# Kernel optimization log

Measured on AMD Instinct MI355X. Metric: run time of the kernel, lower is better.

## Reference

```python
import jax, jax.numpy as jnp
import numpy as np

T, B, D = 2048, 1, 1024
N_HEAD, D_HEAD, D_FF = 16, 64, 4096
LN_EPS = 1e-5


def layer_norm(x, g, b):
    m = jnp.mean(x, axis=-1, keepdims=True)
    v = jnp.mean(jnp.square(x - m), axis=-1, keepdims=True)
    return (x - m) * jax.lax.rsqrt(v + LN_EPS) * g + b


def rel_shift(x):
    # x: (qlen, klen, bsz, n_head) -> Transformer-XL relative shift
    q, k, b, h = x.shape
    zp = jnp.zeros((q, 1, b, h), dtype=x.dtype)
    x = jnp.concatenate([zp, x], axis=1)            # (q, k+1, b, h)
    x = x.reshape(k + 1, q, b, h)[1:].reshape(q, k, b, h)
    return x


def setup_inputs() -> dict:
    key = jax.random.key(0)
    ks = jax.random.split(key, 12)
    s = lambda fan: 1.0 / np.sqrt(fan)
    inp = {
        "input": jax.random.normal(ks[0], (T, B, D), jnp.float32),
        "pos": jax.random.normal(ks[1], (T, 1, D), jnp.float32),
        "r_w_bias": jax.random.normal(ks[2], (N_HEAD, D_HEAD), jnp.float32) * 0.02,
        "r_r_bias": jax.random.normal(ks[3], (N_HEAD, D_HEAD), jnp.float32) * 0.02,
        # causal mask: True = masked (future positions)
        "mask": jnp.triu(jnp.ones((T, T), dtype=bool), k=1),
        "ln1_g": jnp.ones((D,), jnp.float32),
        "ln1_b": jnp.zeros((D,), jnp.float32),
        "qkv_w": jax.random.normal(ks[4], (D, 3 * D), jnp.float32) * s(D),
        "r_w": jax.random.normal(ks[5], (D, D), jnp.float32) * s(D),
        "o_w": jax.random.normal(ks[6], (D, D), jnp.float32) * s(D),
        "ln2_g": jnp.ones((D,), jnp.float32),
        "ln2_b": jnp.zeros((D,), jnp.float32),
        "ff_w1": jax.random.normal(ks[7], (D, D_FF), jnp.float32) * s(D),
        "ff_b1": jnp.zeros((D_FF,), jnp.float32),
        "ff_w2": jax.random.normal(ks[8], (D_FF, D), jnp.float32) * s(D_FF),
        "ff_b2": jnp.zeros((D,), jnp.float32),
    }
    return inp


def reference(input, pos, r_w_bias, r_r_bias, mask, ln1_g, ln1_b, qkv_w, r_w,
              o_w, ln2_g, ln2_b, ff_w1, ff_b1, ff_w2, ff_b2):
    scale = 1.0 / np.sqrt(D_HEAD)
    # preprocess_attn: layernorm
    q_in = layer_norm(input, ln1_g, ln1_b)                      # (T,B,D)
    w_heads = jnp.einsum('tbd,de->tbe', q_in, qkv_w)            # (T,B,3D)
    w_q, w_k, w_v = jnp.split(w_heads, 3, axis=-1)
    w_q = w_q.reshape(T, B, N_HEAD, D_HEAD)
    w_k = w_k.reshape(T, B, N_HEAD, D_HEAD)
    w_v = w_v.reshape(T, B, N_HEAD, D_HEAD)
    r_k = (pos[:, 0] @ r_w).reshape(T, N_HEAD, D_HEAD)          # (T,h,dh)

    AC = jnp.einsum('ibnd,jbnd->ijbn', w_q + r_w_bias, w_k)     # (T,T,B,h)
    BD = rel_shift(jnp.einsum('ibnd,jnd->ijbn', w_q + r_r_bias, r_k))
    score = (AC + BD) * scale
    score = jnp.where(mask[:, :, None, None], jnp.finfo(score.dtype).min, score)
    probs = jax.nn.softmax(score, axis=1)                       # coverage
    attn_vec = jnp.einsum('ijbn,jbnd->ibnd', probs, w_v).reshape(T, B, D)
    attn_out = jnp.einsum('tbd,de->tbe', attn_vec, o_w)
    # postprocess_attn: (dropout=identity) + residual
    x = input + attn_out
    # FFN block: layernorm > linear-relu-linear > residual
    y = layer_norm(x, ln2_g, ln2_b)
    y = jax.nn.relu(jnp.einsum('tbd,df->tbf', y, ff_w1) + ff_b1)
    y = jnp.einsum('tbf,fd->tbd', y, ff_w2) + ff_b2
    x = x + y
    return x, probs
```

## Files before the change

kernel.cpp:

```cpp
#include <hip/hip_runtime.h>
#include <hip/hip_bf16.h>
#include <stdint.h>

using bf16 = __hip_bfloat16;
using short8 = __attribute__((ext_vector_type(8))) short;
using f32x4 = __attribute__((ext_vector_type(4))) float;

#define T_SEQ 2048
#define DMODEL 1024
#define NHEAD 16
#define DHEAD 64
#define DFF 4096

struct __align__(8) bf16x4 { bf16 x, y, z, w; };

__device__ __forceinline__ void async_cp16(const bf16* g, bf16* l) {
  __builtin_amdgcn_global_load_lds(
      (const __attribute__((address_space(1))) uint32_t*)g,
      (__attribute__((address_space(3))) uint32_t*)l, 16, 0, 0);
}

__global__ __launch_bounds__(256) void transpose_cvt(const float* __restrict__ src,
                                                     bf16* __restrict__ dst,
                                                     int R, int C) {
  __shared__ float tile[32][33];
  int bx = blockIdx.x * 32;
  int by = blockIdx.y * 32;
  int tx = threadIdx.x, ty = threadIdx.y;
#pragma unroll
  for (int r = 0; r < 32; r += 8)
    tile[ty + r][tx] = src[(long)(by + ty + r) * C + bx + tx];
  __syncthreads();
#pragma unroll
  for (int r = 0; r < 32; r += 8)
    dst[(long)(bx + ty + r) * R + by + tx] = __float2bfloat16(tile[tx][ty + r]);
}

__global__ __launch_bounds__(256) void cvt_bf16(const float* __restrict__ src,
                                                bf16* __restrict__ dst, int n4) {
  int idx = blockIdx.x * 256 + threadIdx.x;
  if (idx < n4) {
    float4 v = ((const float4*)src)[idx];
    bf16x4 o{__float2bfloat16(v.x), __float2bfloat16(v.y),
             __float2bfloat16(v.z), __float2bfloat16(v.w)};
    ((bf16x4*)dst)[idx] = o;
  }
}

__global__ __launch_bounds__(256) void ln_cvt(const float* __restrict__ x,
                                              const float* __restrict__ g,
                                              const float* __restrict__ b,
                                              bf16* __restrict__ out) {
  int row = blockIdx.x;
  int tid = threadIdx.x;
  float4 v = ((const float4*)(x + (long)row * DMODEL))[tid];
  float s = v.x + v.y + v.z + v.w;
  float s2 = v.x * v.x + v.y * v.y + v.z * v.z + v.w * v.w;
#pragma unroll
  for (int off = 32; off > 0; off >>= 1) {
    s += __shfl_down(s, off);
    s2 += __shfl_down(s2, off);
  }
  __shared__ float ss[4], ss2[4];
  int wave = tid >> 6, lane = tid & 63;
  if (lane == 0) { ss[wave] = s; ss2[wave] = s2; }
  __syncthreads();
  s = ss[0] + ss[1] + ss[2] + ss[3];
  s2 = ss2[0] + ss2[1] + ss2[2] + ss2[3];
  float mean = s * (1.0f / DMODEL);
  float var = s2 * (1.0f / DMODEL) - mean * mean;
  float rstd = rsqrtf(var + 1e-5f);
  float4 gg = ((const float4*)g)[tid];
  float4 bb = ((const float4*)b)[tid];
  bf16x4 o{__float2bfloat16((v.x - mean) * rstd * gg.x + bb.x),
           __float2bfloat16((v.y - mean) * rstd * gg.y + bb.y),
           __float2bfloat16((v.z - mean) * rstd * gg.z + bb.z),
           __float2bfloat16((v.w - mean) * rstd * gg.w + bb.w)};
  ((bf16x4*)(out + (long)row * DMODEL))[tid] = o;
}

template <int BN, class Epi>
__global__ __launch_bounds__(256) void gemm_bt(const bf16* __restrict__ A,
                                               const bf16* __restrict__ Bt,
                                               int M, int N, int K,
                                               long aZstride, long bZstride, Epi epi) {
  constexpr int BM = 128;
  constexpr int BK = 32;
  constexpr int NT = BN / 32;
  __shared__ bf16 As[BM * BK];
  __shared__ bf16 Bs[BN * BK];

  const int bm = blockIdx.y, bn = blockIdx.x, z = blockIdx.z;
  const bf16* Ab = A + (long)z * aZstride;
  const bf16* Bb = Bt + (long)z * bZstride;

  const int tid = threadIdx.x;
  const int lane = tid & 63;
  const int wave = tid >> 6;
  const int wr = wave >> 1;
  const int wc = wave & 1;
  const int kEnd = epi.kmax(bm, bn, K);

  const f32x4 zero4 = {0.f, 0.f, 0.f, 0.f};
  f32x4 acc[4][NT];
#pragma unroll
  for (int mt = 0; mt < 4; ++mt)
#pragma unroll
    for (int nt = 0; nt < NT; ++nt) acc[mt][nt] = zero4;

  const int sr = tid >> 2;
  const int sc = (tid & 3) * 8;
  const bf16* aG0 = Ab + (long)(bm * BM + sr) * K + sc;
  const bf16* aG1 = Ab + (long)(bm * BM + 64 + sr) * K + sc;
  bf16* aL0 = As + tid * 8;
  bf16* aL1 = As + 2048 + tid * 8;
  const bf16* bG0 = Bb + (long)(bn * BN + sr) * K + sc;
  bf16* bL0 = Bs + tid * 8;
  const bf16* bG1 = Bb + (long)(bn * BN + 64 + sr) * K + sc;
  bf16* bL1 = Bs + 2048 + tid * 8;

  const int aRow = wr * 64 + (lane & 15);
  const int bRow = wc * (BN / 2) + (lane & 15);
  const int kq = (lane >> 4) * 8;

  for (int k0 = 0; k0 < kEnd; k0 += BK) {
    __syncthreads();
    async_cp16(aG0, aL0);
    async_cp16(aG1, aL1);
    async_cp16(bG0, bL0);
    if constexpr (BN == 128) async_cp16(bG1, bL1);
    aG0 += BK; aG1 += BK; bG0 += BK;
    if constexpr (BN == 128) bG1 += BK;
    __syncthreads();
    short8 af[4], bfr[NT];
#pragma unroll
    for (int mt = 0; mt < 4; ++mt)
      af[mt] = *(const short8*)(As + (aRow + mt * 16) * BK + kq);
#pragma unroll
    for (int nt = 0; nt < NT; ++nt)
      bfr[nt] = *(const short8*)(Bs + (bRow + nt * 16) * BK + kq);
#pragma unroll
    for (int mt = 0; mt < 4; ++mt)
#pragma unroll
      for (int nt = 0; nt < NT; ++nt)
        acc[mt][nt] = __builtin_amdgcn_mfma_f32_16x16x32_bf16(af[mt], bfr[nt],
                                                              acc[mt][nt], 0, 0, 0);
  }

  const int rBase = (lane >> 4) * 4;
  const int cOff = lane & 15;
#pragma unroll
  for (int mt = 0; mt < 4; ++mt) {
#pragma unroll
    for (int nt = 0; nt < NT; ++nt) {
      int row = bm * BM + wr * 64 + mt * 16 + rBase;
      int col = bn * BN + wc * (BN / 2) + nt * 16 + cOff;
      f32x4 v = acc[mt][nt];
#pragma unroll
      for (int r = 0; r < 4; ++r) epi.store(z, row + r, col, v[r]);
    }
  }
}

struct EpiQKV {
  bf16 *Qh, *Kb, *Vt;
  __device__ int kmax(int, int, int K) const { return K; }
  __device__ void store(int, int row, int col, float v) const {
    int n = (col >> 6) & 15, d = col & 63;
    long hoff = ((long)n * T_SEQ + row) * DHEAD + d;
    if (col < DMODEL) {
      Qh[hoff] = __float2bfloat16(v);
    } else if (col < 2 * DMODEL) {
      Kb[hoff] = __float2bfloat16(v);
    } else {
      Vt[((long)n * DHEAD + d) * T_SEQ + row] = __float2bfloat16(v);
    }
  }
};

struct EpiRk {
  bf16* Rk;
  __device__ int kmax(int, int, int K) const { return K; }
  __device__ void store(int, int row, int col, float v) const {
    int n = col >> 6, d = col & 63;
    Rk[((long)n * T_SEQ + row) * DHEAD + d] = __float2bfloat16(v);
  }
};

struct EpiPV {
  bf16* av;
  __device__ int kmax(int bm, int, int K) const {
    int kl = (bm + 1) * 128;
    return kl < K ? kl : K;
  }
  __device__ void store(int z, int row, int col, float v) const {
    av[(long)row * DMODEL + z * DHEAD + col] = __float2bfloat16(v);
  }
};

struct EpiO {
  float* xws;
  const float* inp;
  __device__ int kmax(int, int, int K) const { return K; }
  __device__ void store(int, int row, int col, float v) const {
    long idx = (long)row * DMODEL + col;
    xws[idx] = v + inp[idx];
  }
};

struct EpiFF1 {
  bf16* h;
  const float* b1;
  __device__ int kmax(int, int, int K) const { return K; }
  __device__ void store(int, int row, int col, float v) const {
    h[(long)row * DFF + col] = __float2bfloat16(fmaxf(v + b1[col], 0.f));
  }
};

struct EpiFF2 {
  float* out;
  const float* b2;
  const float* xws;
  __device__ int kmax(int, int, int K) const { return K; }
  __device__ void store(int, int row, int col, float v) const {
    long idx = (long)row * DMODEL + col;
    out[idx] = v + b2[col] + xws[idx];
  }
};

__global__ __launch_bounds__(256) void bias_k(const bf16* __restrict__ Kb,
                                              const bf16* __restrict__ Rk,
                                              const float* __restrict__ rwb,
                                              const float* __restrict__ rrb,
                                              float* __restrict__ acB,
                                              float* __restrict__ rrbR) {
  int idx = blockIdx.x * 256 + threadIdx.x;
  int n = idx >> 11;
  const short8* kp = (const short8*)(Kb + (long)idx * DHEAD);
  const short8* rp = (const short8*)(Rk + (long)idx * DHEAD);
  float s1 = 0.f, s2 = 0.f;
#pragma unroll
  for (int q8 = 0; q8 < 8; ++q8) {
    short8 kv = kp[q8], rv = rp[q8];
#pragma unroll
    for (int e = 0; e < 8; ++e) {
      float w1 = rwb[n * DHEAD + q8 * 8 + e];
      float w2 = rrb[n * DHEAD + q8 * 8 + e];
      s1 += w1 * __bfloat162float(((const bf16*)&kv)[e]);
      s2 += w2 * __bfloat162float(((const bf16*)&rv)[e]);
    }
  }
  acB[idx] = s1;
  rrbR[idx] = s2;
}

__global__ __launch_bounds__(256) void score_k(const bf16* __restrict__ Qh,
                                               const bf16* __restrict__ Kb,
                                               const bf16* __restrict__ Rk,
                                               const float* __restrict__ acB,
                                               const float* __restrict__ rrbR,
                                               bf16* __restrict__ score) {
  const int bn = blockIdx.x, bm = blockIdx.y, z = blockIdx.z;
  if (bn > bm) return;
  __shared__ char smem[65536];
  bf16* Qs  = (bf16*)smem;
  bf16* Ks  = (bf16*)(smem + 16384);
  bf16* Bnd = (bf16*)(smem + 32768);

  const int tid = threadIdx.x;
  const int lane = tid & 63, wave = tid >> 6;
  const int wr = wave >> 1, wc = wave & 1;
  const int kq = (lane >> 4) * 8;
  const int l15 = lane & 15;
  const int base = 128 * (bn - bm) + T_SEQ - 1 - 128;

  const bf16* Qg = Qh + ((long)z * T_SEQ + bm * 128) * DHEAD;
  const bf16* Kg = Kb + ((long)z * T_SEQ + bn * 128) * DHEAD;
  const bf16* Rg = Rk + (long)z * T_SEQ * DHEAD;

#pragma unroll
  for (int it = 0; it < 4; ++it) {
    int s = it * 256 + tid;
    int kh = s >> 9, r = (s >> 2) & 127, c = (s & 3) * 8;
    async_cp16(Qg + (long)r * DHEAD + kh * 32 + c, Qs + s * 8);
    async_cp16(Kg + (long)r * DHEAD + kh * 32 + c, Ks + s * 8);
  }
#pragma unroll
  for (int it = 0; it < 8; ++it) {
    int s = it * 256 + tid;
    int kh = s >> 10, u = (s >> 2) & 255, c = (s & 3) * 8;
    int g = base + u;
    g = g < 0 ? 0 : (g > T_SEQ - 1 ? T_SEQ - 1 : g);
    async_cp16(Rg + (long)g * DHEAD + kh * 32 + c, Bnd + s * 8);
  }

  const f32x4 zero4 = {0.f, 0.f, 0.f, 0.f};
  f32x4 accA[4][4], accW[4][8];
#pragma unroll
  for (int mt = 0; mt < 4; ++mt) {
#pragma unroll
    for (int nt = 0; nt < 4; ++nt) accA[mt][nt] = zero4;
#pragma unroll
    for (int ut = 0; ut < 8; ++ut) accW[mt][ut] = zero4;
  }

  __syncthreads();
#pragma unroll
  for (int kh = 0; kh < 2; ++kh) {
    short8 qa[4], kf[4], wf[8];
#pragma unroll
    for (int mt = 0; mt < 4; ++mt)
      qa[mt] = *(const short8*)(Qs + kh * 4096 + (wr * 64 + mt * 16 + l15) * 32 + kq);
#pragma unroll
    for (int nt = 0; nt < 4; ++nt)
      kf[nt] = *(const short8*)(Ks + kh * 4096 + (wc * 64 + nt * 16 + l15) * 32 + kq);
#pragma unroll
    for (int ut = 0; ut < 8; ++ut)
      wf[ut] = *(const short8*)(Bnd + kh * 8192 + (wc * 128 + ut * 16 + l15) * 32 + kq);
#pragma unroll
    for (int mt = 0; mt < 4; ++mt) {
#pragma unroll
      for (int nt = 0; nt < 4; ++nt)
        accA[mt][nt] = __builtin_amdgcn_mfma_f32_16x16x32_bf16(qa[mt], kf[nt], accA[mt][nt], 0, 0, 0);
#pragma unroll
      for (int ut = 0; ut < 8; ++ut)
        accW[mt][ut] = __builtin_amdgcn_mfma_f32_16x16x32_bf16(qa[mt], wf[ut], accW[mt][ut], 0, 0, 0);
    }
  }
  __syncthreads();

  float wbias[8];
#pragma unroll
  for (int ut = 0; ut < 8; ++ut) {
    int u = wc * 128 + ut * 16 + l15;
    int g = base + u;
    g = g < 0 ? 0 : (g > T_SEQ - 1 ? T_SEQ - 1 : g);
    wbias[ut] = rrbR[(long)z * T_SEQ + g];
  }
  float abias[4];
#pragma unroll
  for (int nt = 0; nt < 4; ++nt)
    abias[nt] = acB[(long)z * T_SEQ + bn * 128 + wc * 64 + nt * 16 + l15];

  bf16* WlH = (bf16*)smem;
  const int quad4 = (lane >> 4) * 4;
  bf16* srow = score + (long)z * T_SEQ * T_SEQ;

  for (int half = 0; half < 2; ++half) {
    if (wr == half) {
#pragma unroll
      for (int mt = 0; mt < 4; ++mt)
#pragma unroll
        for (int ut = 0; ut < 8; ++ut) {
          int lr = mt * 16 + quad4;
          int u = wc * 128 + ut * 16 + l15;
#pragma unroll
          for (int reg = 0; reg < 4; ++reg)
            WlH[(lr + reg) * 272 + u] = __float2bfloat16(accW[mt][ut][reg] + wbias[ut]);
        }
    }
    __syncthreads();
    if (wr == half) {
#pragma unroll
      for (int mt = 0; mt < 4; ++mt)
#pragma unroll
        for (int nt = 0; nt < 4; ++nt) {
          int lr = mt * 16 + quad4;
          int c = wc * 64 + nt * 16 + l15;
#pragma unroll
          for (int reg = 0; reg < 4; ++reg) {
            int r = half * 64 + lr + reg;
            int u = c - r + 128;
            float v = accA[mt][nt][reg] + abias[nt] +
                      __bfloat162float(WlH[(lr + reg) * 272 + u]);
            srow[(long)(bm * 128 + r) * T_SEQ + bn * 128 + c] = __float2bfloat16(v);
          }
        }
    }
    __syncthreads();
  }
}

__global__ __launch_bounds__(256) void softmax_k(const bf16* __restrict__ S,
                                                 float* __restrict__ probs,
                                                 bf16* __restrict__ pb) {
  constexpr int HS = T_SEQ + 8;
  __shared__ bf16 pl[NHEAD * HS];
  __shared__ float rinv_s[NHEAD];
  const int i = blockIdx.x;
  const int tid = threadIdx.x;
  const int wave = tid >> 6, lane = tid & 63;
  const float scale = 0.125f;
  const int nch = ((i + 1) + 511) >> 9;

  for (int q = 0; q < 4; ++q) {
    const int h = wave * 4 + q;
    const bf16* row = S + (long)h * T_SEQ * T_SEQ + (long)i * T_SEQ;
    float m = -1e30f;
    for (int c = 0; c < nch; ++c) {
      int j0 = c * 512 + lane * 8;
      short8 v = *(const short8*)(row + j0);
#pragma unroll
      for (int e = 0; e < 8; ++e) {
        float s = (j0 + e <= i) ? __bfloat162float(((const bf16*)&v)[e]) * scale : -1e30f;
        m = fmaxf(m, s);
      }
    }
#pragma unroll
    for (int off = 1; off < 64; off <<= 1) m = fmaxf(m, __shfl_xor(m, off));
    float l = 0.f;
    for (int c = 0; c < nch; ++c) {
      int j0 = c * 512 + lane * 8;
      short8 v = *(const short8*)(row + j0);
      short8 o;
#pragma unroll
      for (int e = 0; e < 8; ++e) {
        float p = 0.f;
        if (j0 + e <= i) {
          p = __expf(__bfloat162float(((const bf16*)&v)[e]) * scale - m);
          l += p;
        }
        ((bf16*)&o)[e] = __float2bfloat16(p);
      }
      *(short8*)(pl + h * HS + j0) = o;
    }
#pragma unroll
    for (int off = 1; off < 64; off <<= 1) l += __shfl_xor(l, off);
    if (lane == 0) rinv_s[h] = 1.f / l;
  }
  __syncthreads();

  float* prow = probs + (long)i * T_SEQ * NHEAD;
  const int n0 = (tid & 3) * 4;
  float rv0 = rinv_s[n0 + 0], rv1 = rinv_s[n0 + 1];
  float rv2 = rinv_s[n0 + 2], rv3 = rinv_s[n0 + 3];
  for (int it = 0; it < 32; ++it) {
    int o = tid * 4 + it * 1024;
    int j = o >> 4;
    float4 f = {0.f, 0.f, 0.f, 0.f};
    if (j <= i) {
      f.x = __bfloat162float(pl[(n0 + 0) * HS + j]) * rv0;
      f.y = __bfloat162float(pl[(n0 + 1) * HS + j]) * rv1;
      f.z = __bfloat162float(pl[(n0 + 2) * HS + j]) * rv2;
      f.w = __bfloat162float(pl[(n0 + 3) * HS + j]) * rv3;
    }
    ((float4*)prow)[tid + it * 256] = f;
  }

  const int kround = ((i >> 7) + 1) << 7;
  for (int q = 0; q < 4; ++q) {
    const int h = wave * 4 + q;
    bf16* prow_b = pb + (long)h * T_SEQ * T_SEQ + (long)i * T_SEQ;
    float rinv = rinv_s[h];
    for (int j0 = lane * 8; j0 < kround; j0 += 512) {
      short8 v = *(const short8*)(pl + h * HS + j0);
      short8 o;
#pragma unroll
      for (int e = 0; e < 8; ++e)
        ((bf16*)&o)[e] = __float2bfloat16(__bfloat162float(((const bf16*)&v)[e]) * rinv);
      *(short8*)(prow_b + j0) = o;
    }
  }
}

extern "C" void kernel_launch(void* const* d_in, const int* in_sizes, int n_in,
                              void* d_out, int out_size, void* d_ws, size_t ws_size,
                              hipStream_t stream) {
  const float* input = (const float*)d_in[0];
  const float* pos   = (const float*)d_in[1];
  const float* rwb   = (const float*)d_in[2];
  const float* rrb   = (const float*)d_in[3];
  const float* ln1g  = (const float*)d_in[5];
  const float* ln1b  = (const float*)d_in[6];
  const float* qkvw  = (const float*)d_in[7];
  const float* rw    = (const float*)d_in[8];
  const float* ow    = (const float*)d_in[9];
  const float* ln2g  = (const float*)d_in[10];
  const float* ln2b  = (const float*)d_in[11];
  const float* ffw1  = (const float*)d_in[12];
  const float* ffb1  = (const float*)d_in[13];
  const float* ffw2  = (const float*)d_in[14];
  const float* ffb2  = (const float*)d_in[15];
  float* out = (float*)d_out;

  size_t off = 0;
  auto alloc = [&](size_t bytes) -> char* {
    char* p = (char*)d_ws + off;
    off += (bytes + 255) & ~(size_t)255;
    return p;
  };
  bf16* wqkvT = (bf16*)alloc(3072L * 1024 * 2);
  bf16* wrT   = (bf16*)alloc(1024L * 1024 * 2);
  bf16* woT   = (bf16*)alloc(1024L * 1024 * 2);
  bf16* wf1T  = (bf16*)alloc(4096L * 1024 * 2);
  bf16* wf2T  = (bf16*)alloc(1024L * 4096 * 2);
  bf16* qin   = (bf16*)alloc(2048L * 1024 * 2);
  bf16* posb  = (bf16*)alloc(2048L * 1024 * 2);
  bf16* Qh    = (bf16*)alloc(16L * 2048 * 64 * 2);
  bf16* Kb    = (bf16*)alloc(16L * 2048 * 64 * 2);
  bf16* Vt    = (bf16*)alloc(16L * 64 * 2048 * 2);
  bf16* Rk    = (bf16*)alloc(16L * 2048 * 64 * 2);
  float* acB  = (float*)alloc(16L * 2048 * 4);
  float* rrbR = (float*)alloc(16L * 2048 * 4);
  bf16* ACb   = (bf16*)alloc(16L * 2048 * 2048 * 2);
  bf16* pb    = (bf16*)alloc(16L * 2048 * 2048 * 2);
  bf16* av    = (bf16*)alloc(2048L * 1024 * 2);
  float* xws  = (float*)alloc(2048L * 1024 * 4);
  bf16* yb    = (bf16*)alloc(2048L * 1024 * 2);
  bf16* hb    = (bf16*)alloc(2048L * 4096 * 2);

  dim3 tb(32, 8);
  transpose_cvt<<<dim3(3072 / 32, 1024 / 32), tb, 0, stream>>>(qkvw, wqkvT, 1024, 3072);
  transpose_cvt<<<dim3(1024 / 32, 1024 / 32), tb, 0, stream>>>(rw, wrT, 1024, 1024);
  transpose_cvt<<<dim3(1024 / 32, 1024 / 32), tb, 0, stream>>>(ow, woT, 1024, 1024);
  transpose_cvt<<<dim3(4096 / 32, 1024 / 32), tb, 0, stream>>>(ffw1, wf1T, 1024, 4096);
  transpose_cvt<<<dim3(1024 / 32, 4096 / 32), tb, 0, stream>>>(ffw2, wf2T, 4096, 1024);
  cvt_bf16<<<2048, 256, 0, stream>>>(pos, posb, 2048 * 1024 / 4);
  ln_cvt<<<2048, 256, 0, stream>>>(input, ln1g, ln1b, qin);

  {
    EpiQKV e{Qh, Kb, Vt};
    gemm_bt<128, EpiQKV><<<dim3(24, 16, 1), 256, 0, stream>>>(qin, wqkvT, 2048, 3072, 1024, 0, 0, e);
  }
  {
    EpiRk e{Rk};
    gemm_bt<128, EpiRk><<<dim3(8, 16, 1), 256, 0, stream>>>(posb, wrT, 2048, 1024, 1024, 0, 0, e);
  }
  bias_k<<<128, 256, 0, stream>>>(Kb, Rk, rwb, rrb, acB, rrbR);
  score_k<<<dim3(16, 16, 16), 256, 0, stream>>>(Qh, Kb, Rk, acB, rrbR, ACb);
  softmax_k<<<2048, 256, 0, stream>>>(ACb, out + 2048L * 1024, pb);
  {
    EpiPV e{av};
    gemm_bt<64, EpiPV><<<dim3(1, 16, 16), 256, 0, stream>>>(pb, Vt, 2048, 64, 2048,
                                                            2048L * 2048, 64L * 2048, e);
  }
  {
    EpiO e{xws, input};
    gemm_bt<128, EpiO><<<dim3(8, 16, 1), 256, 0, stream>>>(av, woT, 2048, 1024, 1024, 0, 0, e);
  }
  ln_cvt<<<2048, 256, 0, stream>>>(xws, ln2g, ln2b, yb);
  {
    EpiFF1 e{hb, ffb1};
    gemm_bt<128, EpiFF1><<<dim3(32, 16, 1), 256, 0, stream>>>(yb, wf1T, 2048, 4096, 1024, 0, 0, e);
  }
  {
    EpiFF2 e{out, ffb2, xws};
    gemm_bt<128, EpiFF2><<<dim3(8, 16, 1), 256, 0, stream>>>(hb, wf2T, 2048, 1024, 4096, 0, 0, e);
  }
}
```

Before: 895.1 us.

## Widen softmax to one wave per head, single-pass score epilogue, smaller GEMM tiles

The score kernel's epilogue now stages both row halves of the shifted positional tile in enlarged LDS at once, writing only the needed u-range, which removes the two-phase loop and its extra barriers. Softmax runs 1024 threads per row with one wave per head, keeps the loaded score chunks in registers instead of reading them twice from global memory, and writes the probs output with a contiguous per-thread index. The N=1024 GEMMs (Rk, output projection, FF2) switch to 64-wide tiles with twice as many blocks to fill more CUs. In exchange, LDS use in score_k grows, which can lower occupancy, and the smaller GEMM tiles reuse data less.

Result: faster. 790.1 us (-11.7%).

```diff
diff --git a/kernel.cpp b/kernel.cpp
--- a/kernel.cpp
+++ b/kernel.cpp
@@ -262,7 +262,7 @@
                                                bf16* __restrict__ score) {
   const int bn = blockIdx.x, bm = blockIdx.y, z = blockIdx.z;
   if (bn > bm) return;
-  __shared__ char smem[65536];
+  __shared__ char smem[70656];
   bf16* Qs  = (bf16*)smem;
   bf16* Ks  = (bf16*)(smem + 16384);
   bf16* Bnd = (bf16*)(smem + 32768);
@@ -327,7 +327,6 @@
         accW[mt][ut] = __builtin_amdgcn_mfma_f32_16x16x32_bf16(qa[mt], wf[ut], accW[mt][ut], 0, 0, 0);
     }
   }
-  __syncthreads();
 
   float wbias[8];
 #pragma unroll
@@ -342,101 +341,109 @@
   for (int nt = 0; nt < 4; ++nt)
     abias[nt] = acB[(long)z * T_SEQ + bn * 128 + wc * 64 + nt * 16 + l15];
 
-  bf16* WlH = (bf16*)smem;
+  __syncthreads();
+
+  bf16* Wl = (bf16*)smem + wr * (64 * 276);
   const int quad4 = (lane >> 4) * 4;
+  const int umin = wr ? 1 : 65;
+  const int umax = wr ? 191 : 255;
+#pragma unroll
+  for (int mt = 0; mt < 4; ++mt) {
+#pragma unroll
+    for (int ut = 0; ut < 8; ++ut) {
+      int ub = wc * 128 + ut * 16;
+      if (ub + 15 < umin || ub > umax) continue;
+      int lr = mt * 16 + quad4;
+      int u = ub + l15;
+#pragma unroll
+      for (int reg = 0; reg < 4; ++reg)
+        Wl[(lr + reg) * 276 + u] = __float2bfloat16(accW[mt][ut][reg] + wbias[ut]);
+    }
+  }
+  __syncthreads();
+
   bf16* srow = score + (long)z * T_SEQ * T_SEQ;
-
-  for (int half = 0; half < 2; ++half) {
-    if (wr == half) {
-#pragma unroll
-      for (int mt = 0; mt < 4; ++mt)
-#pragma unroll
-        for (int ut = 0; ut < 8; ++ut) {
-          int lr = mt * 16 + quad4;
-          int u = wc * 128 + ut * 16 + l15;
-#pragma unroll
-          for (int reg = 0; reg < 4; ++reg)
-            WlH[(lr + reg) * 272 + u] = __float2bfloat16(accW[mt][ut][reg] + wbias[ut]);
-        }
-    }
-    __syncthreads();
-    if (wr == half) {
-#pragma unroll
-      for (int mt = 0; mt < 4; ++mt)
-#pragma unroll
-        for (int nt = 0; nt < 4; ++nt) {
-          int lr = mt * 16 + quad4;
-          int c = wc * 64 + nt * 16 + l15;
-#pragma unroll
-          for (int reg = 0; reg < 4; ++reg) {
-            int r = half * 64 + lr + reg;
-            int u = c - r + 128;
-            float v = accA[mt][nt][reg] + abias[nt] +
-                      __bfloat162float(WlH[(lr + reg) * 272 + u]);
-            srow[(long)(bm * 128 + r) * T_SEQ + bn * 128 + c] = __float2bfloat16(v);
-          }
-        }
-    }
-    __syncthreads();
-  }
-}
-
-__global__ __launch_bounds__(256) void softmax_k(const bf16* __restrict__ S,
-                                                 float* __restrict__ probs,
-                                                 bf16* __restrict__ pb) {
+#pragma unroll
+  for (int mt = 0; mt < 4; ++mt) {
+#pragma unroll
+    for (int nt = 0; nt < 4; ++nt) {
+      int lr = mt * 16 + quad4;
+      int c = wc * 64 + nt * 16 + l15;
+#pragma unroll
+      for (int reg = 0; reg < 4; ++reg) {
+        int rl = lr + reg;
+        int r = wr * 64 + rl;
+        int u = c - r + 128;
+        float v = accA[mt][nt][reg] + abias[nt] +
+                  __bfloat162float(Wl[rl * 276 + u]);
+        srow[(long)(bm * 128 + r) * T_SEQ + bn * 128 + c] = __float2bfloat16(v);
+      }
+    }
+  }
+}
+
+__global__ __launch_bounds__(1024) void softmax_k(const bf16* __restrict__ S,
+                                                  float* __restrict__ probs,
+                                                  bf16* __restrict__ pb) {
   constexpr int HS = T_SEQ + 8;
   __shared__ bf16 pl[NHEAD * HS];
   __shared__ float rinv_s[NHEAD];
   const int i = blockIdx.x;
   const int tid = threadIdx.x;
-  const int wave = tid >> 6, lane = tid & 63;
+  const int h = tid >> 6, lane = tid & 63;
   const float scale = 0.125f;
-  const int nch = ((i + 1) + 511) >> 9;
-
-  for (int q = 0; q < 4; ++q) {
-    const int h = wave * 4 + q;
-    const bf16* row = S + (long)h * T_SEQ * T_SEQ + (long)i * T_SEQ;
-    float m = -1e30f;
-    for (int c = 0; c < nch; ++c) {
+  const int nch = (i >> 9) + 1;
+
+  const bf16* row = S + (long)h * T_SEQ * T_SEQ + (long)i * T_SEQ;
+
+  short8 v[4];
+  float m = -1e30f;
+#pragma unroll
+  for (int c = 0; c < 4; ++c) {
+    if (c < nch) {
       int j0 = c * 512 + lane * 8;
-      short8 v = *(const short8*)(row + j0);
+      v[c] = *(const short8*)(row + j0);
 #pragma unroll
       for (int e = 0; e < 8; ++e) {
-        float s = (j0 + e <= i) ? __bfloat162float(((const bf16*)&v)[e]) * scale : -1e30f;
+        float s = (j0 + e <= i) ? __bfloat162float(((const bf16*)&v[c])[e]) * scale : -1e30f;
         m = fmaxf(m, s);
       }
     }
-#pragma unroll
-    for (int off = 1; off < 64; off <<= 1) m = fmaxf(m, __shfl_xor(m, off));
-    float l = 0.f;
-    for (int c = 0; c < nch; ++c) {
+  }
+#pragma unroll
+  for (int off = 1; off < 64; off <<= 1) m = fmaxf(m, __shfl_xor(m, off));
+
+  float l = 0.f;
+#pragma unroll
+  for (int c = 0; c < 4; ++c) {
+    if (c < nch) {
       int j0 = c * 512 + lane * 8;
-      short8 v = *(const short8*)(row + j0);
       short8 o;
 #pragma unroll
       for (int e = 0; e < 8; ++e) {
         float p = 0.f;
         if (j0 + e <= i) {
-          p = __expf(__bfloat162float(((const bf16*)&v)[e]) * scale - m);
+          p = __expf(__bfloat162float(((const bf16*)&v[c])[e]) * scale - m);
           l += p;
         }
         ((bf16*)&o)[e] = __float2bfloat16(p);
       }
       *(short8*)(pl + h * HS + j0) = o;
     }
-#pragma unroll
-    for (int off = 1; off < 64; off <<= 1) l += __shfl_xor(l, off);
-    if (lane == 0) rinv_s[h] = 1.f / l;
-  }
+  }
+#pragma unroll
+  for (int off = 1; off < 64; off <<= 1) l += __shfl_xor(l, off);
+  if (lane == 0) rinv_s[h] = 1.f / l;
   __syncthreads();
 
   float* prow = probs + (long)i * T_SEQ * NHEAD;
   const int n0 = (tid & 3) * 4;
-  float rv0 = rinv_s[n0 + 0], rv1 = rinv_s[n0 + 1];
-  float rv2 = rinv_s[n0 + 2], rv3 = rinv_s[n0 + 3];
-  for (int it = 0; it < 32; ++it) {
-    int o = tid * 4 + it * 1024;
-    int j = o >> 4;
+  const float rv0 = rinv_s[n0 + 0], rv1 = rinv_s[n0 + 1];
+  const float rv2 = rinv_s[n0 + 2], rv3 = rinv_s[n0 + 3];
+#pragma unroll
+  for (int it = 0; it < 8; ++it) {
+    int o = it * 1024 + tid;
+    int j = o >> 2;
     float4 f = {0.f, 0.f, 0.f, 0.f};
     if (j <= i) {
       f.x = __bfloat162float(pl[(n0 + 0) * HS + j]) * rv0;
@@ -444,22 +451,19 @@
       f.z = __bfloat162float(pl[(n0 + 2) * HS + j]) * rv2;
       f.w = __bfloat162float(pl[(n0 + 3) * HS + j]) * rv3;
     }
-    ((float4*)prow)[tid + it * 256] = f;
+    ((float4*)prow)[o] = f;
   }
 
   const int kround = ((i >> 7) + 1) << 7;
-  for (int q = 0; q < 4; ++q) {
-    const int h = wave * 4 + q;
-    bf16* prow_b = pb + (long)h * T_SEQ * T_SEQ + (long)i * T_SEQ;
-    float rinv = rinv_s[h];
-    for (int j0 = lane * 8; j0 < kround; j0 += 512) {
-      short8 v = *(const short8*)(pl + h * HS + j0);
-      short8 o;
-#pragma unroll
-      for (int e = 0; e < 8; ++e)
-        ((bf16*)&o)[e] = __float2bfloat16(__bfloat162float(((const bf16*)&v)[e]) * rinv);
-      *(short8*)(prow_b + j0) = o;
-    }
+  bf16* prow_b = pb + (long)h * T_SEQ * T_SEQ + (long)i * T_SEQ;
+  const float rinv = rinv_s[h];
+  for (int j0 = lane * 8; j0 < kround; j0 += 512) {
+    short8 pv = *(const short8*)(pl + h * HS + j0);
+    short8 o;
+#pragma unroll
+    for (int e = 0; e < 8; ++e)
+      ((bf16*)&o)[e] = __float2bfloat16(__bfloat162float(((const bf16*)&pv)[e]) * rinv);
+    *(short8*)(prow_b + j0) = o;
   }
 }
 
@@ -524,11 +528,11 @@
   }
   {
     EpiRk e{Rk};
-    gemm_bt<128, EpiRk><<<dim3(8, 16, 1), 256, 0, stream>>>(posb, wrT, 2048, 1024, 1024, 0, 0, e);
+    gemm_bt<64, EpiRk><<<dim3(16, 16, 1), 256, 0, stream>>>(posb, wrT, 2048, 1024, 1024, 0, 0, e);
   }
   bias_k<<<128, 256, 0, stream>>>(Kb, Rk, rwb, rrb, acB, rrbR);
   score_k<<<dim3(16, 16, 16), 256, 0, stream>>>(Qh, Kb, Rk, acB, rrbR, ACb);
-  softmax_k<<<2048, 256, 0, stream>>>(ACb, out + 2048L * 1024, pb);
+  softmax_k<<<2048, 1024, 0, stream>>>(ACb, out + 2048L * 1024, pb);
   {
     EpiPV e{av};
     gemm_bt<64, EpiPV><<<dim3(1, 16, 16), 256, 0, stream>>>(pb, Vt, 2048, 64, 2048,
@@ -536,7 +540,7 @@
   }
   {
     EpiO e{xws, input};
-    gemm_bt<128, EpiO><<<dim3(8, 16, 1), 256, 0, stream>>>(av, woT, 2048, 1024, 1024, 0, 0, e);
+    gemm_bt<64, EpiO><<<dim3(16, 16, 1), 256, 0, stream>>>(av, woT, 2048, 1024, 1024, 0, 0, e);
   }
   ln_cvt<<<2048, 256, 0, stream>>>(xws, ln2g, ln2b, yb);
   {
@@ -545,6 +549,6 @@
   }
   {
     EpiFF2 e{out, ffb2, xws};
-    gemm_bt<128, EpiFF2><<<dim3(8, 16, 1), 256, 0, stream>>>(hb, wf2T, 2048, 1024, 4096, 0, 0, e);
-  }
-}
+    gemm_bt<64, EpiFF2><<<dim3(16, 16, 1), 256, 0, stream>>>(hb, wf2T, 2048, 1024, 4096, 0, 0, e);
+  }
+}
```
